# Kernel optimization log

Measured on AMD Instinct MI355X. Metric: run time of the kernel, lower is better.

## Reference

```python
import jax, jax.numpy as jnp
import numpy as np

B, T, D = 256, 512, 128   # batch, T_max, input_dim
Z, TR, EM, RH = 128, 256, 256, 512  # z_dim, trans_dim, emission_dim, rnn_dim


def _dkf_infer(x, y, eps_comb, eps_emit, rnn_Wih, rnn_Whh, rnn_bih, rnn_bhh, h0, zq0,
               tr_g1_W, tr_g1_b, tr_g2_W, tr_g2_b, tr_p1_W, tr_p1_b, tr_p2_W, tr_p2_b,
               tr_mu_W, tr_mu_b, tr_lv_W, tr_lv_b,
               cb_h_W, cb_h_b, cb_mu_W, cb_mu_b, cb_lv_W, cb_lv_b,
               em_h1_W, em_h1_b, em_h2_W, em_h2_b, em_mu_W, em_mu_b, em_logvar):
    b = x.shape[0]
    # --- nn.RNN (relu nonlinearity, batch_first), scanned time-major ---
    xw = jnp.einsum('btd,dh->tbh', x, rnn_Wih) + rnn_bih  # [T,B,RH] input projection hoisted out of scan

    def rnn_step(h, xw_t):
        h = jax.nn.relu(xw_t + h @ rnn_Whh + rnn_bhh)
        return h, h

    _, rnn_out = jax.lax.scan(rnn_step, jnp.broadcast_to(h0, (b, h0.shape[0])), xw)  # [T,B,RH]

    y_tm = jnp.swapaxes(y, 0, 1)  # [T,B,D]

    def step(z_prev, inp):
        h_rnn, yt, e_cb, e_em = inp
        # GatedTransition (infer only uses prior mu/logvar; its sample is discarded)
        gate = jax.nn.sigmoid(jax.nn.relu(z_prev @ tr_g1_W + tr_g1_b) @ tr_g2_W + tr_g2_b)
        prop = jax.nn.relu(z_prev @ tr_p1_W + tr_p1_b) @ tr_p2_W + tr_p2_b
        pr_mu = (1.0 - gate) * (z_prev @ tr_mu_W + tr_mu_b) + gate * prop
        pr_lv = jax.nn.relu(prop) @ tr_lv_W + tr_lv_b
        # Combiner + reparameterization
        hc = 0.5 * (jnp.tanh(z_prev @ cb_h_W + cb_h_b) + h_rnn)
        mu = hc @ cb_mu_W + cb_mu_b
        lv = hc @ cb_lv_W + cb_lv_b
        z_t = mu + e_cb * jnp.exp(0.5 * lv)
        # Emitter + reparameterization
        h1 = jax.nn.relu(z_t @ em_h1_W + em_h1_b)
        h2 = jax.nn.relu(h1 @ em_h2_W + em_h2_b)
        x_mu = h2 @ em_mu_W + em_mu_b
        x_t = x_mu + e_em * jnp.exp(0.5 * em_logvar)
        # KL(q || prior) summed over z, per batch element
        kl = jnp.sum(0.5 * (pr_lv - lv + (jnp.exp(lv) + (mu - pr_mu) ** 2) / jnp.exp(pr_lv) - 1.0), axis=1)
        # per-element MSE reduced over x_dim
        rec = jnp.mean((x_t - yt) ** 2, axis=1)
        return z_t, (kl, rec)

    z0 = jnp.broadcast_to(zq0, (b, zq0.shape[0]))
    _, (kl_states, rec_losses) = jax.lax.scan(step, z0, (rnn_out, y_tm, eps_comb, eps_emit))
    return jnp.stack([jnp.mean(rec_losses), jnp.mean(kl_states)])  # [rec_loss, kl_loss]


def setup_inputs() -> dict:
    key = jax.random.key(0)
    ks = iter(jax.random.split(key, 32))
    nrm = lambda shape, s=0.05: jax.random.normal(next(ks), shape, dtype=jnp.float32) * s
    z = lambda *shape: jnp.zeros(shape, jnp.float32)
    return dict(
        x=nrm((B, T, D), 1.0), y=nrm((B, T, D), 1.0),
        eps_comb=nrm((T, B, Z), 1.0), eps_emit=nrm((T, B, D), 1.0),
        rnn_Wih=nrm((D, RH)), rnn_Whh=nrm((RH, RH)), rnn_bih=z(RH), rnn_bhh=z(RH),
        h0=z(RH), zq0=z(Z),
        tr_g1_W=nrm((Z, TR)), tr_g1_b=z(TR), tr_g2_W=nrm((TR, Z)), tr_g2_b=z(Z),
        tr_p1_W=nrm((Z, TR)), tr_p1_b=z(TR), tr_p2_W=nrm((TR, Z)), tr_p2_b=z(Z),
        tr_mu_W=jnp.eye(Z, dtype=jnp.float32), tr_mu_b=z(Z),  # identity init as in torch code
        tr_lv_W=nrm((Z, Z)), tr_lv_b=z(Z),
        cb_h_W=nrm((Z, RH)), cb_h_b=z(RH),
        cb_mu_W=nrm((RH, Z)), cb_mu_b=z(Z),
        cb_lv_W=nrm((RH, Z)), cb_lv_b=z(Z),
        em_h1_W=nrm((Z, EM)), em_h1_b=z(EM),
        em_h2_W=nrm((EM, EM)), em_h2_b=z(EM),
        em_mu_W=nrm((EM, D)), em_mu_b=z(D),
        em_logvar=jnp.ones((D,), jnp.float32),  # nn.Parameter(torch.ones(input_dim))
    )


def reference(x, y, eps_comb, eps_emit, rnn_Wih, rnn_Whh, rnn_bih, rnn_bhh, h0, zq0,
              tr_g1_W, tr_g1_b, tr_g2_W, tr_g2_b, tr_p1_W, tr_p1_b, tr_p2_W, tr_p2_b,
              tr_mu_W, tr_mu_b, tr_lv_W, tr_lv_b,
              cb_h_W, cb_h_b, cb_mu_W, cb_mu_b, cb_lv_W, cb_lv_b,
              em_h1_W, em_h1_b, em_h2_W, em_h2_b, em_mu_W, em_mu_b, em_logvar):
    return _dkf_infer(x, y, eps_comb, eps_emit, rnn_Wih, rnn_Whh, rnn_bih, rnn_bhh, h0, zq0,
                      tr_g1_W, tr_g1_b, tr_g2_W, tr_g2_b, tr_p1_W, tr_p1_b, tr_p2_W, tr_p2_b,
                      tr_mu_W, tr_mu_b, tr_lv_W, tr_lv_b,
                      cb_h_W, cb_h_b, cb_mu_W, cb_mu_b, cb_lv_W, cb_lv_b,
                      em_h1_W, em_h1_b, em_h2_W, em_h2_b, em_mu_W, em_mu_b, em_logvar)
```

## Files before the change

kernel.cpp:

```cpp
#include <hip/hip_runtime.h>


#define T_LEN 512
#define BATCH 256
#define DIMX  128
#define ZDIM  128
#define RHD   512
#define CHUNK 32

typedef _Float16 f16;
typedef _Float16 f16x4 __attribute__((ext_vector_type(4)));
typedef _Float16 f16x8 __attribute__((ext_vector_type(8)));
typedef float    f32x4 __attribute__((ext_vector_type(4)));

#define MFMA16(a,b,c) __builtin_amdgcn_mfma_f32_16x16x32_f16((a),(b),(c),0,0,0)

#define PK_WIH  0u
#define PK_WHH  65536u
#define PK_G1   327680u
#define PK_G2   360448u
#define PK_P1   393216u
#define PK_P2   425984u
#define PK_TMU  458752u
#define PK_TLV  475136u
#define PK_CBH  491520u
#define PK_CBML 557056u
#define PK_E1   688128u
#define PK_E2   720896u
#define PK_EMU  786432u

#define WS_XW   0ull
#define WS_Z    (WS_XW  + 134217728ull)
#define WS_MU   (WS_Z   + 33619968ull)
#define WS_LV   (WS_MU  + 33554432ull)
#define WS_PK   (WS_LV  + 33554432ull)
#define WS_PART (WS_PK  + 1638400ull)
#define WS_PROG (WS_PART + 16384ull)
#define WS_END  (WS_PROG + 256ull)

__device__ __forceinline__ void ldsfence() {
  asm volatile("s_waitcnt lgkmcnt(0)" ::: "memory");
  __builtin_amdgcn_sched_barrier(0);
}

__device__ __forceinline__ void lbar() {
  asm volatile("s_waitcnt lgkmcnt(0)" ::: "memory");
  __builtin_amdgcn_s_barrier();
  asm volatile("" ::: "memory");
}

__device__ __forceinline__ void pin8(f16x8& v) {
  f32x4 t = __builtin_bit_cast(f32x4, v);
  asm volatile("" : "+v"(t));
  v = __builtin_bit_cast(f16x8, t);
}

template<int N>
__device__ __forceinline__ void zacc(f32x4* a) {
  f32x4 z = {0.f, 0.f, 0.f, 0.f};
#pragma unroll
  for (int i = 0; i < N; ++i) a[i] = z;
}

__device__ __forceinline__ f16x8 cvt8(const float* p) {
  float4 a = *(const float4*)p, b = *(const float4*)(p + 4);
  f16x8 r;
  r[0] = (f16)a.x; r[1] = (f16)a.y; r[2] = (f16)a.z; r[3] = (f16)a.w;
  r[4] = (f16)b.x; r[5] = (f16)b.y; r[6] = (f16)b.z; r[7] = (f16)b.w;
  return r;
}

__device__ __forceinline__ int swz(int row, int col) {
  return (row << 9) + (col ^ ((row & 7) << 3));
}
__device__ __forceinline__ int swz128(int row, int col) {
  return (row << 7) + (col ^ ((row & 7) << 3));
}

template<int KS>
__device__ __forceinline__ void load_af(const f16* src, int sstr, int lane, f16x8* af) {
#pragma unroll
  for (int ks = 0; ks < KS; ++ks)
    af[ks] = *(const f16x8*)(src + (lane & 15) * sstr + ks * 32 + ((lane >> 4) << 3));
}

template<int KS, int NT>
__device__ __forceinline__ void gemm_regA(const f16x8* af, const f16* __restrict__ bp,
                                          int lane, f32x4* acc) {
#pragma unroll
  for (int ks = 0; ks < KS; ++ks)
#pragma unroll
    for (int j = 0; j < NT; ++j) {
      f16x8 bf = *(const f16x8*)(bp + (((size_t)(ks * NT + j)) << 9) + (lane << 3));
      acc[j] = MFMA16(af[ks], bf, acc[j]);
    }
}

template<int NT>
__device__ __forceinline__ void store_relu(const f32x4* acc, const float* __restrict__ bias,
                                           f16* dst, int dstr, int lane) {
  int colv = lane & 15, rb = (lane >> 4) << 2;
#pragma unroll
  for (int j = 0; j < NT; ++j)
#pragma unroll
    for (int r = 0; r < 4; ++r)
      dst[(rb + r) * dstr + j * 16 + colv] = (f16)fmaxf(acc[j][r] + bias[j * 16 + colv], 0.f);
}

struct PackEnt { const float* s1; const float* s2; int nsplit, K, N; unsigned dst, wg0; };
struct PackTab { PackEnt e[13]; };

__global__ void pack_all_kernel(PackTab tb, f16* __restrict__ pk) {
  int i = 0;
#pragma unroll
  for (int k = 1; k < 13; ++k)
    if (blockIdx.x >= tb.e[k].wg0) i = k;
  const PackEnt& E = tb.e[i];
  int idx = (blockIdx.x - E.wg0) * 256 + threadIdx.x;
  if (idx >= E.K * E.N) return;
  int j = idx & 7, l = (idx >> 3) & 63, fi = idx >> 9;
  int NTt = E.N >> 4;
  int nt = fi % NTt, ks = fi / NTt;
  int k = ks * 32 + ((l >> 4) << 3) + j;
  int n = (nt << 4) + (l & 15);
  float v;
  if (n < E.nsplit) v = E.s1[(size_t)k * E.nsplit + n];
  else              v = E.s2[(size_t)k * (E.N - E.nsplit) + (n - E.nsplit)];
  pk[E.dst + idx] = (f16)v;
}

__global__ void zero_prog_kernel(unsigned* __restrict__ p) {
  if (threadIdx.x < 16)
    __hip_atomic_store(p + threadIdx.x, 0u, __ATOMIC_RELAXED, __HIP_MEMORY_SCOPE_AGENT);
}

__global__ __launch_bounds__(256) void xw_kernel(
    const float* __restrict__ x, const f16* __restrict__ pk,
    const float* __restrict__ bih, const float* __restrict__ bhh,
    f16* __restrict__ xw) {
  __shared__ float bs[512];
  const int tid = threadIdx.x, lane = tid & 63, w = tid >> 6;
  const int colv = lane & 15, l4 = lane >> 4;
  const int m0 = blockIdx.x * 64 + w * 16;
  const int t = m0 >> 8, b0 = m0 & 255;
  for (int i = tid; i < 512; i += 256) bs[i] = bih[i] + bhh[i];
  __syncthreads();
  f16x8 xB[4];
  const float* xr = x + ((size_t)(b0 + colv) * T_LEN + t) * DIMX;
#pragma unroll
  for (int ks = 0; ks < 4; ++ks) xB[ks] = cvt8(xr + ks * 32 + l4 * 8);
  f32x4 acc[32]; zacc<32>(acc);
#pragma unroll
  for (int ks = 0; ks < 4; ++ks)
#pragma unroll
    for (int mt = 0; mt < 32; ++mt)
      acc[mt] = MFMA16(*(const f16x8*)(pk + PK_WIH + ((size_t)(ks * 32 + mt) << 9) + (lane << 3)),
                       xB[ks], acc[mt]);
  f16* xo = xw + ((size_t)t * BATCH + b0 + colv) * RHD;
#pragma unroll
  for (int mt = 0; mt < 32; ++mt) {
    f16x4 v;
#pragma unroll
    for (int r = 0; r < 4; ++r) v[r] = (f16)(acc[mt][r] + bs[mt * 16 + l4 * 4 + r]);
    *(f16x4*)(xo + mt * 16 + l4 * 4) = v;
  }
}

__global__ __launch_bounds__(256, 1) void scan_pipe_kernel(
    const f16* __restrict__ pk, const float* __restrict__ h0,
    const float* __restrict__ zq0, const float* __restrict__ chb,
    const float* __restrict__ cmb, const float* __restrict__ clb,
    const float* __restrict__ eps_comb, f16* __restrict__ xw,
    f16* __restrict__ z_all, f16* __restrict__ mu_all, f16* __restrict__ lv_all,
    unsigned* __restrict__ prog) {
  __shared__ __align__(16) f16 lds[73728];
  const int tid = threadIdx.x, lane = tid & 63, w = tid >> 6;
  const int colv = lane & 15, l4 = lane >> 4;

  if (blockIdx.x < 16) {
    const int g = blockIdx.x, b0 = g * 16;
    f16* whh_lds = lds;
    f16* h_st = lds + 65536;
    {
      const uint4* src = (const uint4*)(pk + PK_WHH + 196608u);
      for (int i = tid; i < 8192; i += 256) ((uint4*)whh_lds)[i] = src[i];
    }
    f16x8 whhA[8][12];
#pragma unroll
    for (int mt = 0; mt < 8; ++mt)
#pragma unroll
      for (int ks = 0; ks < 12; ++ks) {
        whhA[mt][ks] = *(const f16x8*)(pk + PK_WHH +
            ((size_t)(ks * 32 + w * 8 + mt) << 9) + (lane << 3));
        pin8(whhA[mt][ks]);
      }
    for (int i = tid; i < 8192; i += 256) h_st[swz(i >> 9, i & 511)] = (f16)h0[i & 511];
    __syncthreads();

    const int moff = w * 128 + l4 * 4;
    f16* xp = xw + (size_t)(b0 + colv) * RHD;
    f16x4 xwc[8], xwn[8];
#pragma unroll
    for (int mt = 0; mt < 8; ++mt) xwc[mt] = *(const f16x4*)(xp + moff + mt * 16);

    for (int c = 0; c < T_LEN / CHUNK; ++c) {
#pragma unroll 1
      for (int tt = 0; tt < CHUNK; ++tt) {
        int t = c * CHUNK + tt;
        f16* xpn = (t < T_LEN - 1) ? xp + (size_t)BATCH * RHD : xp;
#pragma unroll
        for (int mt = 0; mt < 8; ++mt) xwn[mt] = *(const f16x4*)(xpn + moff + mt * 16);
        f32x4 acc[8]; zacc<8>(acc);
#pragma unroll
        for (int ks = 0; ks < 12; ++ks) {
          f16x8 B = *(const f16x8*)&h_st[swz(colv, ks * 32 + l4 * 8)];
#pragma unroll
          for (int mt = 0; mt < 8; ++mt) acc[mt] = MFMA16(whhA[mt][ks], B, acc[mt]);
        }
#pragma unroll
        for (int ks = 0; ks < 4; ++ks) {
          f16x8 B = *(const f16x8*)&h_st[swz(colv, (12 + ks) * 32 + l4 * 8)];
#pragma unroll
          for (int mt = 0; mt < 8; ++mt)
            acc[mt] = MFMA16(*(const f16x8*)(whh_lds +
                (((ks * 32 + w * 8 + mt) << 6) + lane) * 8), B, acc[mt]);
        }
        lbar();
#pragma unroll
        for (int mt = 0; mt < 8; ++mt) {
          f16x4 h4;
#pragma unroll
          for (int r = 0; r < 4; ++r)
            h4[r] = (f16)fmaxf(acc[mt][r] + (float)xwc[mt][r], 0.f);
          *(f16x4*)&h_st[swz(colv, moff + mt * 16)] = h4;
          *(f16x4*)(xp + moff + mt * 16) = h4;
        }
        lbar();
        xp = xpn;
#pragma unroll
        for (int mt = 0; mt < 8; ++mt) xwc[mt] = xwn[mt];
      }
      __syncthreads();
      if (tid == 0)
        __hip_atomic_store(prog + g, (unsigned)(c + 1), __ATOMIC_RELEASE,
                           __HIP_MEMORY_SCOPE_AGENT);
    }
  } else {
    const int g = blockIdx.x - 16, b0 = g * 16;
    f16* cbml_lds = lds;
    f16* hc_st = lds + 32768;
    f16* z_st  = lds + 40960;
    f16* m_st  = lds + 43008;
    {
      const uint4* src = (const uint4*)(pk + PK_CBML + 98304u);
      for (int i = tid; i < 4096; i += 256) ((uint4*)cbml_lds)[i] = src[i];
    }
    f16x8 cbhA[8][4];
#pragma unroll
    for (int mt = 0; mt < 8; ++mt)
#pragma unroll
      for (int ks = 0; ks < 4; ++ks) {
        cbhA[mt][ks] = *(const f16x8*)(pk + PK_CBH +
            ((size_t)(ks * 32 + w * 8 + mt) << 9) + (lane << 3));
        pin8(cbhA[mt][ks]);
      }
    f16x8 cbmlA[4][12];
#pragma unroll
    for (int mt = 0; mt < 4; ++mt)
#pragma unroll
      for (int ks = 0; ks < 12; ++ks) {
        cbmlA[mt][ks] = *(const f16x8*)(pk + PK_CBML +
            ((size_t)(ks * 16 + w * 4 + mt) << 9) + (lane << 3));
        pin8(cbmlA[mt][ks]);
      }
    f16x4 chbv[8];
#pragma unroll
    for (int mt = 0; mt < 8; ++mt)
#pragma unroll
      for (int r = 0; r < 4; ++r)
        chbv[mt][r] = (f16)chb[(w * 8 + mt) * 16 + l4 * 4 + r];
    float mb[4][4];
#pragma unroll
    for (int mt = 0; mt < 4; ++mt)
#pragma unroll
      for (int r = 0; r < 4; ++r) {
        int d = (w * 4 + mt) * 16 + l4 * 4 + r;
        mb[mt][r] = (d < 128) ? cmb[d] : clb[d - 128];
      }
    for (int i = tid; i < 2048; i += 256) {
      f16 zv = (f16)zq0[i & 127];
      z_st[swz128(i >> 7, i & 127)] = zv;
      z_all[(size_t)(b0 + (i >> 7)) * ZDIM + (i & 127)] = zv;
    }
    __syncthreads();

    const int moff = w * 128 + l4 * 4;
    const int m2off = w * 64 + l4 * 4;
    const int be = tid >> 4, d0 = (tid & 15) * 8;
    const f16* hp = xw + (size_t)(b0 + colv) * RHD;
    const float* epb = eps_comb + (size_t)(b0 + be) * ZDIM + d0;
    f16x4 hv[8];
    float4 ep0, ep1, epn0, epn1;

    for (int c = 0; c < T_LEN / CHUNK; ++c) {
      if (tid == 0) {
        while (__hip_atomic_load(prog + g, __ATOMIC_RELAXED,
                                 __HIP_MEMORY_SCOPE_AGENT) < (unsigned)(c + 1))
          __builtin_amdgcn_s_sleep(2);
      }
      __syncthreads();
      __builtin_amdgcn_fence(__ATOMIC_ACQUIRE, "agent");
      {
        const f16* hpt = hp + (size_t)(c * CHUNK) * BATCH * RHD;
#pragma unroll
        for (int mt = 0; mt < 8; ++mt) hv[mt] = *(const f16x4*)(hpt + moff + mt * 16);
        const float* ept = epb + (size_t)(c * CHUNK) * BATCH * ZDIM;
        ep0 = *(const float4*)ept; ep1 = *(const float4*)(ept + 4);
      }
#pragma unroll 1
      for (int tt = 0; tt < CHUNK; ++tt) {
        int t = c * CHUNK + tt;
        f16x8 zB[4];
#pragma unroll
        for (int ks = 0; ks < 4; ++ks)
          zB[ks] = *(const f16x8*)&z_st[swz128(colv, ks * 32 + l4 * 8)];
        f32x4 a1[8]; zacc<8>(a1);
#pragma unroll
        for (int ks = 0; ks < 4; ++ks)
#pragma unroll
          for (int mt = 0; mt < 8; ++mt) a1[mt] = MFMA16(cbhA[mt][ks], zB[ks], a1[mt]);
#pragma unroll
        for (int mt = 0; mt < 8; ++mt) {
          f16x4 hc4;
#pragma unroll
          for (int r = 0; r < 4; ++r) {
            float cs = a1[mt][r] + (float)chbv[mt][r];
            float ex = __builtin_amdgcn_exp2f(cs * 2.885390082f);
            float th = 1.f - 2.f * __builtin_amdgcn_rcpf(ex + 1.f);
            hc4[r] = (f16)(0.5f * (th + (float)hv[mt][r]));
          }
          *(f16x4*)&hc_st[swz(colv, moff + mt * 16)] = hc4;
        }
        lbar();
        if (tt < CHUNK - 1) {
          const f16* hpt = hp + (size_t)(t + 1) * BATCH * RHD;
#pragma unroll
          for (int mt = 0; mt < 8; ++mt) hv[mt] = *(const f16x4*)(hpt + moff + mt * 16);
          const float* ept = epb + (size_t)(t + 1) * BATCH * ZDIM;
          epn0 = *(const float4*)ept; epn1 = *(const float4*)(ept + 4);
        }
        f32x4 a2[4]; zacc<4>(a2);
#pragma unroll
        for (int ks = 0; ks < 12; ++ks) {
          f16x8 hcB = *(const f16x8*)&hc_st[swz(colv, ks * 32 + l4 * 8)];
#pragma unroll
          for (int mt = 0; mt < 4; ++mt) a2[mt] = MFMA16(cbmlA[mt][ks], hcB, a2[mt]);
        }
#pragma unroll
        for (int ks = 0; ks < 4; ++ks) {
          f16x8 hcB = *(const f16x8*)&hc_st[swz(colv, (12 + ks) * 32 + l4 * 8)];
#pragma unroll
          for (int mt = 0; mt < 4; ++mt)
            a2[mt] = MFMA16(*(const f16x8*)(cbml_lds +
                (((ks * 16 + w * 4 + mt) << 6) + lane) * 8), hcB, a2[mt]);
        }
#pragma unroll
        for (int mt = 0; mt < 4; ++mt) {
          f16x4 v;
#pragma unroll
          for (int r = 0; r < 4; ++r) v[r] = (f16)(a2[mt][r] + mb[mt][r]);
          *(f16x4*)&m_st[colv * 264 + m2off + mt * 16] = v;
        }
        lbar();
        {
          f16x8 mu8 = *(const f16x8*)&m_st[be * 264 + d0];
          f16x8 lv8 = *(const f16x8*)&m_st[be * 264 + 128 + d0];
          float epv[8] = {ep0.x, ep0.y, ep0.z, ep0.w, ep1.x, ep1.y, ep1.z, ep1.w};
          f16x8 z8;
#pragma unroll
          for (int r = 0; r < 8; ++r) {
            float mu = (float)mu8[r], lv = (float)lv8[r];
            z8[r] = (f16)(mu + epv[r] * __builtin_amdgcn_exp2f(lv * 0.7213475204f));
          }
          *(f16x8*)&z_st[swz128(be, d0)] = z8;
          size_t o = ((size_t)t * BATCH + b0 + be) * ZDIM + d0;
          *(f16x8*)(z_all + o + (size_t)BATCH * ZDIM) = z8;
          *(f16x8*)(mu_all + o) = mu8;
          *(f16x8*)(lv_all + o) = lv8;
        }
        lbar();
        ep0 = epn0; ep1 = epn1;
      }
    }
  }
}

__global__ __launch_bounds__(256) void dpar_kernel(
    const f16* __restrict__ z_all, const f16* __restrict__ mu_all,
    const f16* __restrict__ lv_all, const float* __restrict__ y,
    const float* __restrict__ eps_emit, const f16* __restrict__ pk,
    const float* __restrict__ g1b, const float* __restrict__ g2b,
    const float* __restrict__ p1b, const float* __restrict__ p2b,
    const float* __restrict__ tmub, const float* __restrict__ tlvb,
    const float* __restrict__ e1b, const float* __restrict__ e2b,
    const float* __restrict__ emub, const float* __restrict__ em_logvar,
    float* __restrict__ partials) {
  __shared__ __align__(16) f16 sb256[4][16 * 264];
  __shared__ __align__(16) f16 sb128[4][16 * 136];
  __shared__ float wsum[4][2];
  const int tid = threadIdx.x, lane = tid & 63, w = tid >> 6;
  const int colv = lane & 15, rb = (lane >> 4) << 2;
  const int m0 = blockIdx.x * 64 + w * 16;
  const int t = m0 >> 8, b0 = m0 & 255;
  f16* B256 = &sb256[w][0];
  f16* B128 = &sb128[w][0];

  f16x8 zp[4], zt[4];
  const f16* zpr = z_all + ((size_t)t * BATCH + b0) * ZDIM;
#pragma unroll
  for (int ks = 0; ks < 4; ++ks) {
    zp[ks] = *(const f16x8*)(zpr + (size_t)colv * ZDIM + ks * 32 + ((lane >> 4) << 3));
    zt[ks] = *(const f16x8*)(zpr + (size_t)BATCH * ZDIM + (size_t)colv * ZDIM + ks * 32 + ((lane >> 4) << 3));
  }

  f32x4 a16[16], a8[8];
  f16x8 af[8], af4[4];
  zacc<16>(a16); gemm_regA<4, 16>(zp, pk + PK_G1, lane, a16);
  store_relu<16>(a16, g1b, B256, 264, lane); ldsfence();
  load_af<8>(B256, 264, lane, af); ldsfence();
  zacc<8>(a8); gemm_regA<8, 8>(af, pk + PK_G2, lane, a8);
  f32x4 gate[8];
#pragma unroll
  for (int j = 0; j < 8; ++j)
#pragma unroll
    for (int r = 0; r < 4; ++r)
      gate[j][r] = 1.f / (1.f + expf(-(a8[j][r] + g2b[j * 16 + colv])));
  zacc<16>(a16); gemm_regA<4, 16>(zp, pk + PK_P1, lane, a16);
  store_relu<16>(a16, p1b, B256, 264, lane); ldsfence();
  load_af<8>(B256, 264, lane, af); ldsfence();
  zacc<8>(a8); gemm_regA<8, 8>(af, pk + PK_P2, lane, a8);
  f32x4 prop[8];
#pragma unroll
  for (int j = 0; j < 8; ++j)
#pragma unroll
    for (int r = 0; r < 4; ++r) {
      float v = a8[j][r] + p2b[j * 16 + colv];
      prop[j][r] = v;
      B128[(rb + r) * 136 + j * 16 + colv] = (f16)fmaxf(v, 0.f);
    }
  ldsfence();
  zacc<8>(a8); gemm_regA<4, 8>(zp, pk + PK_TMU, lane, a8);
  f32x4 prmu[8];
#pragma unroll
  for (int j = 0; j < 8; ++j)
#pragma unroll
    for (int r = 0; r < 4; ++r) {
      float gg = gate[j][r];
      prmu[j][r] = (1.f - gg) * (a8[j][r] + tmub[j * 16 + colv]) + gg * prop[j][r];
    }
  load_af<4>(B128, 136, lane, af4); ldsfence();
  zacc<8>(a8); gemm_regA<4, 8>(af4, pk + PK_TLV, lane, a8);
  f32x4 prlv[8];
#pragma unroll
  for (int j = 0; j < 8; ++j)
#pragma unroll
    for (int r = 0; r < 4; ++r) prlv[j][r] = a8[j][r] + tlvb[j * 16 + colv];
  zacc<16>(a16); gemm_regA<4, 16>(zt, pk + PK_E1, lane, a16);
  store_relu<16>(a16, e1b, B256, 264, lane); ldsfence();
  load_af<8>(B256, 264, lane, af); ldsfence();
  zacc<16>(a16); gemm_regA<8, 16>(af, pk + PK_E2, lane, a16);
  store_relu<16>(a16, e2b, B256, 264, lane); ldsfence();
  load_af<8>(B256, 264, lane, af); ldsfence();
  zacc<8>(a8); gemm_regA<8, 8>(af, pk + PK_EMU, lane, a8);
  float srec = 0.f, skl = 0.f;
#pragma unroll
  for (int j = 0; j < 8; ++j)
#pragma unroll
    for (int r = 0; r < 4; ++r) {
      int row = rb + r, n = j * 16 + colv;
      size_t tb = (size_t)t * BATCH + b0 + row;
      float xt = a8[j][r] + emub[n] + eps_emit[tb * DIMX + n] * expf(0.5f * em_logvar[n]);
      float dy = xt - y[((size_t)(b0 + row) * T_LEN + t) * DIMX + n];
      srec += dy * dy;
      float m_ = (float)mu_all[tb * ZDIM + n], l_ = (float)lv_all[tb * ZDIM + n];
      float dm = m_ - prmu[j][r];
      skl += 0.5f * (prlv[j][r] - l_ + (expf(l_) + dm * dm) * expf(-prlv[j][r]) - 1.f);
    }
#pragma unroll
  for (int off = 32; off; off >>= 1) {
    srec += __shfl_xor(srec, off);
    skl += __shfl_xor(skl, off);
  }
  if (lane == 0) { wsum[w][0] = srec; wsum[w][1] = skl; }
  __syncthreads();
  if (tid == 0) {
    partials[blockIdx.x * 2 + 0] = wsum[0][0] + wsum[1][0] + wsum[2][0] + wsum[3][0];
    partials[blockIdx.x * 2 + 1] = wsum[0][1] + wsum[1][1] + wsum[2][1] + wsum[3][1];
  }
}

__global__ void finalize_kernel(const float* __restrict__ partials, float* __restrict__ out) {
  __shared__ float sm[256][2];
  int tid = threadIdx.x;
  float r = 0.f, kk = 0.f;
  for (int i = tid; i < 2048; i += 256) {
    r += partials[2 * i];
    kk += partials[2 * i + 1];
  }
  sm[tid][0] = r; sm[tid][1] = kk;
  __syncthreads();
  for (int off = 128; off; off >>= 1) {
    if (tid < off) { sm[tid][0] += sm[tid + off][0]; sm[tid][1] += sm[tid + off][1]; }
    __syncthreads();
  }
  if (tid == 0) {
    out[0] = sm[0][0] / (131072.f * 128.f);
    out[1] = sm[0][1] / 131072.f;
  }
}

extern "C" void kernel_launch(void* const* d_in, const int* in_sizes, int n_in,
                              void* d_out, int out_size, void* d_ws, size_t ws_size,
                              hipStream_t stream) {
  (void)in_sizes; (void)n_in; (void)out_size;
  const float* x        = (const float*)d_in[0];
  const float* y        = (const float*)d_in[1];
  const float* eps_comb = (const float*)d_in[2];
  const float* eps_emit = (const float*)d_in[3];
  const float* wih = (const float*)d_in[4];
  const float* whh = (const float*)d_in[5];
  const float* bih = (const float*)d_in[6];
  const float* bhh = (const float*)d_in[7];
  const float* h0  = (const float*)d_in[8];
  const float* zq0 = (const float*)d_in[9];
  const float* g1W = (const float*)d_in[10]; const float* g1b = (const float*)d_in[11];
  const float* g2W = (const float*)d_in[12]; const float* g2b = (const float*)d_in[13];
  const float* p1W = (const float*)d_in[14]; const float* p1b = (const float*)d_in[15];
  const float* p2W = (const float*)d_in[16]; const float* p2b = (const float*)d_in[17];
  const float* tmuW = (const float*)d_in[18]; const float* tmub = (const float*)d_in[19];
  const float* tlvW = (const float*)d_in[20]; const float* tlvb = (const float*)d_in[21];
  const float* chW = (const float*)d_in[22]; const float* chb = (const float*)d_in[23];
  const float* cmW = (const float*)d_in[24]; const float* cmb = (const float*)d_in[25];
  const float* clW = (const float*)d_in[26]; const float* clb = (const float*)d_in[27];
  const float* e1W = (const float*)d_in[28]; const float* e1b = (const float*)d_in[29];
  const float* e2W = (const float*)d_in[30]; const float* e2b = (const float*)d_in[31];
  const float* emW = (const float*)d_in[32]; const float* emb = (const float*)d_in[33];
  const float* elv = (const float*)d_in[34];

  char* ws = (char*)d_ws;
  f16*  xw      = (f16*)(ws + WS_XW);
  f16*  z_all   = (f16*)(ws + WS_Z);
  f16*  mu_all  = (f16*)(ws + WS_MU);
  f16*  lv_all  = (f16*)(ws + WS_LV);
  f16*  pk      = (f16*)(ws + WS_PK);
  float* partials = (float*)(ws + WS_PART);
  unsigned* prog  = (unsigned*)(ws + WS_PROG);
  float* out = (float*)d_out;
  if (ws_size < WS_END) return;

  zero_prog_kernel<<<dim3(1), dim3(32), 0, stream>>>(prog);

  PackTab tb;
  unsigned wg = 0; int ei = 0;
#define PACK(S1, S2, NS_, K_, N_, OFF) \
  tb.e[ei] = PackEnt{S1, S2, NS_, K_, N_, OFF, wg}; wg += (unsigned)((K_) * (N_)) / 256; ++ei;
  PACK(wih, wih, 512, 128, 512, PK_WIH);
  PACK(whh, whh, 512, 512, 512, PK_WHH);
  PACK(g1W, g1W, 256, 128, 256, PK_G1);
  PACK(g2W, g2W, 128, 256, 128, PK_G2);
  PACK(p1W, p1W, 256, 128, 256, PK_P1);
  PACK(p2W, p2W, 128, 256, 128, PK_P2);
  PACK(tmuW, tmuW, 128, 128, 128, PK_TMU);
  PACK(tlvW, tlvW, 128, 128, 128, PK_TLV);
  PACK(chW, chW, 512, 128, 512, PK_CBH);
  PACK(cmW, clW, 128, 512, 256, PK_CBML);
  PACK(e1W, e1W, 256, 128, 256, PK_E1);
  PACK(e2W, e2W, 256, 256, 256, PK_E2);
  PACK(emW, emW, 128, 256, 128, PK_EMU);
#undef PACK
  pack_all_kernel<<<dim3(wg), dim3(256), 0, stream>>>(tb, pk);

  xw_kernel<<<dim3(2048), dim3(256), 0, stream>>>(x, pk, bih, bhh, xw);
  scan_pipe_kernel<<<dim3(32), dim3(256), 0, stream>>>(
      pk, h0, zq0, chb, cmb, clb, eps_comb, xw, z_all, mu_all, lv_all, prog);
  dpar_kernel<<<dim3(2048), dim3(256), 0, stream>>>(z_all, mu_all, lv_all, y, eps_emit, pk,
                                                    g1b, g2b, p1b, p2b, tmub, tlvb, e1b, e2b,
                                                    emb, elv, partials);
  finalize_kernel<<<dim3(1), dim3(256), 0, stream>>>(partials, out);
}
```

Baseline: 2.523 ms.

## Fuse RNN input projection into scan kernel as flag-synchronized producer blocks

Removes the separate xw_kernel launch and adds 32 producer blocks to the persistent scan kernel. These blocks compute the input projection chunk by chunk and signal completion through per-chunk atomic counters. The RNN blocks wait on those counters one chunk ahead, and the producers throttle on the RNN progress flags because the RNN overwrites xw in place. The aim is to hide the input projection behind the sequential scan, at the cost of more spin-wait synchronization and a dependence on all 64 blocks being co-resident.

```diff
diff --git a/kernel.cpp b/kernel.cpp
--- a/kernel.cpp
+++ b/kernel.cpp
@@ -105,6 +105,10 @@
 #pragma unroll
     for (int r = 0; r < 4; ++r)
       dst[(rb + r) * dstr + j * 16 + colv] = (f16)fmaxf(acc[j][r] + bias[j * 16 + colv], 0.f);
+}
+
+__device__ __forceinline__ unsigned ldflag(const unsigned* p) {
+  return __hip_atomic_load(p, __ATOMIC_RELAXED, __HIP_MEMORY_SCOPE_AGENT);
 }
 
 struct PackEnt { const float* s1; const float* s2; int nsplit, K, N; unsigned dst, wg0; };
@@ -130,40 +134,8 @@
 }
 
 __global__ void zero_prog_kernel(unsigned* __restrict__ p) {
-  if (threadIdx.x < 16)
+  if (threadIdx.x < 64)
     __hip_atomic_store(p + threadIdx.x, 0u, __ATOMIC_RELAXED, __HIP_MEMORY_SCOPE_AGENT);
-}
-
-__global__ __launch_bounds__(256) void xw_kernel(
-    const float* __restrict__ x, const f16* __restrict__ pk,
-    const float* __restrict__ bih, const float* __restrict__ bhh,
-    f16* __restrict__ xw) {
-  __shared__ float bs[512];
-  const int tid = threadIdx.x, lane = tid & 63, w = tid >> 6;
-  const int colv = lane & 15, l4 = lane >> 4;
-  const int m0 = blockIdx.x * 64 + w * 16;
-  const int t = m0 >> 8, b0 = m0 & 255;
-  for (int i = tid; i < 512; i += 256) bs[i] = bih[i] + bhh[i];
-  __syncthreads();
-  f16x8 xB[4];
-  const float* xr = x + ((size_t)(b0 + colv) * T_LEN + t) * DIMX;
-#pragma unroll
-  for (int ks = 0; ks < 4; ++ks) xB[ks] = cvt8(xr + ks * 32 + l4 * 8);
-  f32x4 acc[32]; zacc<32>(acc);
-#pragma unroll
-  for (int ks = 0; ks < 4; ++ks)
-#pragma unroll
-    for (int mt = 0; mt < 32; ++mt)
-      acc[mt] = MFMA16(*(const f16x8*)(pk + PK_WIH + ((size_t)(ks * 32 + mt) << 9) + (lane << 3)),
-                       xB[ks], acc[mt]);
-  f16* xo = xw + ((size_t)t * BATCH + b0 + colv) * RHD;
-#pragma unroll
-  for (int mt = 0; mt < 32; ++mt) {
-    f16x4 v;
-#pragma unroll
-    for (int r = 0; r < 4; ++r) v[r] = (f16)(acc[mt][r] + bs[mt * 16 + l4 * 4 + r]);
-    *(f16x4*)(xo + mt * 16 + l4 * 4) = v;
-  }
 }
 
 __global__ __launch_bounds__(256, 1) void scan_pipe_kernel(
@@ -172,10 +144,13 @@
     const float* __restrict__ cmb, const float* __restrict__ clb,
     const float* __restrict__ eps_comb, f16* __restrict__ xw,
     f16* __restrict__ z_all, f16* __restrict__ mu_all, f16* __restrict__ lv_all,
-    unsigned* __restrict__ prog) {
+    const float* __restrict__ x, const float* __restrict__ bih,
+    const float* __restrict__ bhh, unsigned* __restrict__ flags) {
   __shared__ __align__(16) f16 lds[73728];
   const int tid = threadIdx.x, lane = tid & 63, w = tid >> 6;
   const int colv = lane & 15, l4 = lane >> 4;
+  unsigned* prog = flags;
+  unsigned* xcnt = flags + 32;
 
   if (blockIdx.x < 16) {
     const int g = blockIdx.x, b0 = g * 16;
@@ -197,6 +172,10 @@
     for (int i = tid; i < 8192; i += 256) h_st[swz(i >> 9, i & 511)] = (f16)h0[i & 511];
     __syncthreads();
 
+    if (tid == 0) { while (ldflag(xcnt + 0) < 128u) __builtin_amdgcn_s_sleep(2); }
+    __syncthreads();
+    __builtin_amdgcn_fence(__ATOMIC_ACQUIRE, "agent");
+
     const int moff = w * 128 + l4 * 4;
     f16* xp = xw + (size_t)(b0 + colv) * RHD;
     f16x4 xwc[8], xwn[8];
@@ -204,6 +183,10 @@
     for (int mt = 0; mt < 8; ++mt) xwc[mt] = *(const f16x4*)(xp + moff + mt * 16);
 
     for (int c = 0; c < T_LEN / CHUNK; ++c) {
+      const int cw = (c + 1 < T_LEN / CHUNK) ? c + 1 : T_LEN / CHUNK - 1;
+      if (tid == 0) { while (ldflag(xcnt + cw) < 128u) __builtin_amdgcn_s_sleep(2); }
+      __syncthreads();
+      __builtin_amdgcn_fence(__ATOMIC_ACQUIRE, "agent");
 #pragma unroll 1
       for (int tt = 0; tt < CHUNK; ++tt) {
         int t = c * CHUNK + tt;
@@ -245,7 +228,7 @@
         __hip_atomic_store(prog + g, (unsigned)(c + 1), __ATOMIC_RELEASE,
                            __HIP_MEMORY_SCOPE_AGENT);
     }
-  } else {
+  } else if (blockIdx.x < 32) {
     const int g = blockIdx.x - 16, b0 = g * 16;
     f16* cbml_lds = lds;
     f16* hc_st = lds + 32768;
@@ -304,9 +287,7 @@
 
     for (int c = 0; c < T_LEN / CHUNK; ++c) {
       if (tid == 0) {
-        while (__hip_atomic_load(prog + g, __ATOMIC_RELAXED,
-                                 __HIP_MEMORY_SCOPE_AGENT) < (unsigned)(c + 1))
-          __builtin_amdgcn_s_sleep(2);
+        while (ldflag(prog + g) < (unsigned)(c + 1)) __builtin_amdgcn_s_sleep(2);
       }
       __syncthreads();
       __builtin_amdgcn_fence(__ATOMIC_ACQUIRE, "agent");
@@ -390,6 +371,53 @@
         }
         lbar();
         ep0 = epn0; ep1 = epn1;
+      }
+    }
+  } else {
+    const int p = blockIdx.x - 32;
+    float* bs = (float*)lds;
+    for (int i = tid; i < 512; i += 256) bs[i] = bih[i] + bhh[i];
+    __syncthreads();
+    for (int c = 0; c < T_LEN / CHUNK; ++c) {
+      if (c > 2) {
+        if (tid == 0) {
+          for (;;) {
+            unsigned mn = 0xffffffffu;
+            for (int g2 = 0; g2 < 16; ++g2) mn = min(mn, ldflag(prog + g2));
+            if (mn >= (unsigned)(c - 2)) break;
+            __builtin_amdgcn_s_sleep(32);
+          }
+        }
+        __syncthreads();
+      }
+#pragma unroll 1
+      for (int q = 0; q < 4; ++q) {
+        const int i = c * 128 + p * 4 + q;
+        const int m0 = i * 64 + w * 16;
+        const int t = m0 >> 8, b0 = m0 & 255;
+        f16x8 xB[4];
+        const float* xr = x + ((size_t)(b0 + colv) * T_LEN + t) * DIMX;
+#pragma unroll
+        for (int ks = 0; ks < 4; ++ks) xB[ks] = cvt8(xr + ks * 32 + l4 * 8);
+        f32x4 acc[32]; zacc<32>(acc);
+#pragma unroll
+        for (int ks = 0; ks < 4; ++ks)
+#pragma unroll
+          for (int mt = 0; mt < 32; ++mt)
+            acc[mt] = MFMA16(*(const f16x8*)(pk + PK_WIH +
+                ((size_t)(ks * 32 + mt) << 9) + (lane << 3)), xB[ks], acc[mt]);
+        f16* xo = xw + ((size_t)t * BATCH + b0 + colv) * RHD;
+#pragma unroll
+        for (int mt = 0; mt < 32; ++mt) {
+          f16x4 v;
+#pragma unroll
+          for (int r = 0; r < 4; ++r) v[r] = (f16)(acc[mt][r] + bs[mt * 16 + l4 * 4 + r]);
+          *(f16x4*)(xo + mt * 16 + l4 * 4) = v;
+        }
+        __syncthreads();
+        if (tid == 0)
+          __hip_atomic_fetch_add(xcnt + c, 1u, __ATOMIC_RELEASE,
+                                 __HIP_MEMORY_SCOPE_AGENT);
       }
     }
   }
@@ -554,11 +582,11 @@
   f16*  lv_all  = (f16*)(ws + WS_LV);
   f16*  pk      = (f16*)(ws + WS_PK);
   float* partials = (float*)(ws + WS_PART);
-  unsigned* prog  = (unsigned*)(ws + WS_PROG);
+  unsigned* flags = (unsigned*)(ws + WS_PROG);
   float* out = (float*)d_out;
   if (ws_size < WS_END) return;
 
-  zero_prog_kernel<<<dim3(1), dim3(32), 0, stream>>>(prog);
+  zero_prog_kernel<<<dim3(1), dim3(64), 0, stream>>>(flags);
 
   PackTab tb;
   unsigned wg = 0; int ei = 0;
@@ -580,9 +608,9 @@
 #undef PACK
   pack_all_kernel<<<dim3(wg), dim3(256), 0, stream>>>(tb, pk);
 
-  xw_kernel<<<dim3(2048), dim3(256), 0, stream>>>(x, pk, bih, bhh, xw);
-  scan_pipe_kernel<<<dim3(32), dim3(256), 0, stream>>>(
-      pk, h0, zq0, chb, cmb, clb, eps_comb, xw, z_all, mu_all, lv_all, prog);
+  scan_pipe_kernel<<<dim3(64), dim3(256), 0, stream>>>(
+      pk, h0, zq0, chb, cmb, clb, eps_comb, xw, z_all, mu_all, lv_all,
+      x, bih, bhh, flags);
   dpar_kernel<<<dim3(2048), dim3(256), 0, stream>>>(z_all, mu_all, lv_all, y, eps_emit, pk,
                                                     g1b, g2b, p1b, p2b, tmub, tlvb, e1b, e2b,
                                                     emb, elv, partials);
```

After: 2.550 ms. No clear change (+1.1%).

## Double-buffer RNN hidden state, shrink chunk size, persistent-weight xw kernel

Applied to the files above, without the earlier changes.

The RNN recurrence now ping-pongs the hidden state between two LDS buffers, which removes one workgroup barrier per timestep. One more K-slice of Whh is kept in registers (13 instead of 12), so the LDS-resident part shrinks. The chunk size is halved so the consumer blocks get progress signals sooner and overlap more closely with the producer. The xw projection kernel becomes persistent: 256 blocks keep their Wih slice in registers and loop over tiles, instead of 2048 blocks each reloading all of Wih. The trade-off is higher register pressure and twice as many flag handshakes.

```diff
diff --git a/kernel.cpp b/kernel.cpp
--- a/kernel.cpp
+++ b/kernel.cpp
@@ -6,7 +6,8 @@
 #define DIMX  128
 #define ZDIM  128
 #define RHD   512
-#define CHUNK 32
+#define CHUNK 16
+#define NCHNK 32
 
 typedef _Float16 f16;
 typedef _Float16 f16x4 __attribute__((ext_vector_type(4)));
@@ -105,6 +106,10 @@
 #pragma unroll
     for (int r = 0; r < 4; ++r)
       dst[(rb + r) * dstr + j * 16 + colv] = (f16)fmaxf(acc[j][r] + bias[j * 16 + colv], 0.f);
+}
+
+__device__ __forceinline__ unsigned ldflag(const unsigned* p) {
+  return __hip_atomic_load(p, __ATOMIC_RELAXED, __HIP_MEMORY_SCOPE_AGENT);
 }
 
 struct PackEnt { const float* s1; const float* s2; int nsplit, K, N; unsigned dst, wg0; };
@@ -130,7 +135,7 @@
 }
 
 __global__ void zero_prog_kernel(unsigned* __restrict__ p) {
-  if (threadIdx.x < 16)
+  if (threadIdx.x < 64)
     __hip_atomic_store(p + threadIdx.x, 0u, __ATOMIC_RELAXED, __HIP_MEMORY_SCOPE_AGENT);
 }
 
@@ -141,28 +146,38 @@
   __shared__ float bs[512];
   const int tid = threadIdx.x, lane = tid & 63, w = tid >> 6;
   const int colv = lane & 15, l4 = lane >> 4;
-  const int m0 = blockIdx.x * 64 + w * 16;
-  const int t = m0 >> 8, b0 = m0 & 255;
   for (int i = tid; i < 512; i += 256) bs[i] = bih[i] + bhh[i];
+  f16x8 wihA[8][4];
+#pragma unroll
+  for (int mt = 0; mt < 8; ++mt)
+#pragma unroll
+    for (int ks = 0; ks < 4; ++ks) {
+      wihA[mt][ks] = *(const f16x8*)(pk + PK_WIH +
+          ((size_t)(ks * 32 + w * 8 + mt) << 9) + (lane << 3));
+      pin8(wihA[mt][ks]);
+    }
   __syncthreads();
-  f16x8 xB[4];
-  const float* xr = x + ((size_t)(b0 + colv) * T_LEN + t) * DIMX;
-#pragma unroll
-  for (int ks = 0; ks < 4; ++ks) xB[ks] = cvt8(xr + ks * 32 + l4 * 8);
-  f32x4 acc[32]; zacc<32>(acc);
-#pragma unroll
-  for (int ks = 0; ks < 4; ++ks)
-#pragma unroll
-    for (int mt = 0; mt < 32; ++mt)
-      acc[mt] = MFMA16(*(const f16x8*)(pk + PK_WIH + ((size_t)(ks * 32 + mt) << 9) + (lane << 3)),
-                       xB[ks], acc[mt]);
-  f16* xo = xw + ((size_t)t * BATCH + b0 + colv) * RHD;
-#pragma unroll
-  for (int mt = 0; mt < 32; ++mt) {
-    f16x4 v;
-#pragma unroll
-    for (int r = 0; r < 4; ++r) v[r] = (f16)(acc[mt][r] + bs[mt * 16 + l4 * 4 + r]);
-    *(f16x4*)(xo + mt * 16 + l4 * 4) = v;
+#pragma unroll 1
+  for (int i = blockIdx.x; i < 8192; i += 256) {
+    const int t = i >> 4, b0 = (i & 15) * 16;
+    f16x8 xB[4];
+    const float* xr = x + ((size_t)(b0 + colv) * T_LEN + t) * DIMX;
+#pragma unroll
+    for (int ks = 0; ks < 4; ++ks) xB[ks] = cvt8(xr + ks * 32 + l4 * 8);
+    f32x4 acc[8]; zacc<8>(acc);
+#pragma unroll
+    for (int ks = 0; ks < 4; ++ks)
+#pragma unroll
+      for (int mt = 0; mt < 8; ++mt)
+        acc[mt] = MFMA16(wihA[mt][ks], xB[ks], acc[mt]);
+    f16* xo = xw + ((size_t)t * BATCH + b0 + colv) * RHD + w * 128;
+#pragma unroll
+    for (int mt = 0; mt < 8; ++mt) {
+      f16x4 v;
+#pragma unroll
+      for (int r = 0; r < 4; ++r) v[r] = (f16)(acc[mt][r] + bs[w * 128 + mt * 16 + l4 * 4 + r]);
+      *(f16x4*)(xo + mt * 16 + l4 * 4) = v;
+    }
   }
 }
 
@@ -173,28 +188,28 @@
     const float* __restrict__ eps_comb, f16* __restrict__ xw,
     f16* __restrict__ z_all, f16* __restrict__ mu_all, f16* __restrict__ lv_all,
     unsigned* __restrict__ prog) {
-  __shared__ __align__(16) f16 lds[73728];
+  __shared__ __align__(16) f16 lds[65536];
   const int tid = threadIdx.x, lane = tid & 63, w = tid >> 6;
   const int colv = lane & 15, l4 = lane >> 4;
 
   if (blockIdx.x < 16) {
     const int g = blockIdx.x, b0 = g * 16;
     f16* whh_lds = lds;
-    f16* h_st = lds + 65536;
+    f16* h_db = lds + 49152;
     {
-      const uint4* src = (const uint4*)(pk + PK_WHH + 196608u);
-      for (int i = tid; i < 8192; i += 256) ((uint4*)whh_lds)[i] = src[i];
-    }
-    f16x8 whhA[8][12];
+      const uint4* src = (const uint4*)(pk + PK_WHH + 212992u);
+      for (int i = tid; i < 6144; i += 256) ((uint4*)whh_lds)[i] = src[i];
+    }
+    f16x8 whhA[8][13];
 #pragma unroll
     for (int mt = 0; mt < 8; ++mt)
 #pragma unroll
-      for (int ks = 0; ks < 12; ++ks) {
+      for (int ks = 0; ks < 13; ++ks) {
         whhA[mt][ks] = *(const f16x8*)(pk + PK_WHH +
             ((size_t)(ks * 32 + w * 8 + mt) << 9) + (lane << 3));
         pin8(whhA[mt][ks]);
       }
-    for (int i = tid; i < 8192; i += 256) h_st[swz(i >> 9, i & 511)] = (f16)h0[i & 511];
+    for (int i = tid; i < 8192; i += 256) h_db[swz(i >> 9, i & 511)] = (f16)h0[i & 511];
     __syncthreads();
 
     const int moff = w * 128 + l4 * 4;
@@ -203,36 +218,37 @@
 #pragma unroll
     for (int mt = 0; mt < 8; ++mt) xwc[mt] = *(const f16x4*)(xp + moff + mt * 16);
 
-    for (int c = 0; c < T_LEN / CHUNK; ++c) {
+    for (int c = 0; c < NCHNK; ++c) {
 #pragma unroll 1
       for (int tt = 0; tt < CHUNK; ++tt) {
         int t = c * CHUNK + tt;
+        f16* hr = h_db + (t & 1) * 8192;
+        f16* hw = h_db + ((t & 1) ^ 1) * 8192;
         f16* xpn = (t < T_LEN - 1) ? xp + (size_t)BATCH * RHD : xp;
 #pragma unroll
         for (int mt = 0; mt < 8; ++mt) xwn[mt] = *(const f16x4*)(xpn + moff + mt * 16);
         f32x4 acc[8]; zacc<8>(acc);
 #pragma unroll
-        for (int ks = 0; ks < 12; ++ks) {
-          f16x8 B = *(const f16x8*)&h_st[swz(colv, ks * 32 + l4 * 8)];
+        for (int ks = 0; ks < 13; ++ks) {
+          f16x8 B = *(const f16x8*)&hr[swz(colv, ks * 32 + l4 * 8)];
 #pragma unroll
           for (int mt = 0; mt < 8; ++mt) acc[mt] = MFMA16(whhA[mt][ks], B, acc[mt]);
         }
 #pragma unroll
-        for (int ks = 0; ks < 4; ++ks) {
-          f16x8 B = *(const f16x8*)&h_st[swz(colv, (12 + ks) * 32 + l4 * 8)];
+        for (int ks = 0; ks < 3; ++ks) {
+          f16x8 B = *(const f16x8*)&hr[swz(colv, (13 + ks) * 32 + l4 * 8)];
 #pragma unroll
           for (int mt = 0; mt < 8; ++mt)
             acc[mt] = MFMA16(*(const f16x8*)(whh_lds +
                 (((ks * 32 + w * 8 + mt) << 6) + lane) * 8), B, acc[mt]);
         }
-        lbar();
 #pragma unroll
         for (int mt = 0; mt < 8; ++mt) {
           f16x4 h4;
 #pragma unroll
           for (int r = 0; r < 4; ++r)
             h4[r] = (f16)fmaxf(acc[mt][r] + (float)xwc[mt][r], 0.f);
-          *(f16x4*)&h_st[swz(colv, moff + mt * 16)] = h4;
+          *(f16x4*)&hw[swz(colv, moff + mt * 16)] = h4;
           *(f16x4*)(xp + moff + mt * 16) = h4;
         }
         lbar();
@@ -302,11 +318,9 @@
     f16x4 hv[8];
     float4 ep0, ep1, epn0, epn1;
 
-    for (int c = 0; c < T_LEN / CHUNK; ++c) {
+    for (int c = 0; c < NCHNK; ++c) {
       if (tid == 0) {
-        while (__hip_atomic_load(prog + g, __ATOMIC_RELAXED,
-                                 __HIP_MEMORY_SCOPE_AGENT) < (unsigned)(c + 1))
-          __builtin_amdgcn_s_sleep(2);
+        while (ldflag(prog + g) < (unsigned)(c + 1)) __builtin_amdgcn_s_sleep(2);
       }
       __syncthreads();
       __builtin_amdgcn_fence(__ATOMIC_ACQUIRE, "agent");
@@ -558,7 +572,7 @@
   float* out = (float*)d_out;
   if (ws_size < WS_END) return;
 
-  zero_prog_kernel<<<dim3(1), dim3(32), 0, stream>>>(prog);
+  zero_prog_kernel<<<dim3(1), dim3(64), 0, stream>>>(prog);
 
   PackTab tb;
   unsigned wg = 0; int ei = 0;
@@ -580,7 +594,7 @@
 #undef PACK
   pack_all_kernel<<<dim3(wg), dim3(256), 0, stream>>>(tb, pk);
 
-  xw_kernel<<<dim3(2048), dim3(256), 0, stream>>>(x, pk, bih, bhh, xw);
+  xw_kernel<<<dim3(256), dim3(256), 0, stream>>>(x, pk, bih, bhh, xw);
   scan_pipe_kernel<<<dim3(32), dim3(256), 0, stream>>>(
       pk, h0, zq0, chb, cmb, clb, eps_comb, xw, z_all, mu_all, lv_all, prog);
   dpar_kernel<<<dim3(2048), dim3(256), 0, stream>>>(z_all, mu_all, lv_all, y, eps_emit, pk,
```

Result: slower. 2.822 ms (+11.9%).
